# Optimization experiments

Measured on AMD Instinct MI355X. Metric: run time of the kernel, lower is better.

## Reference

```python
import jax, jax.numpy as jnp
import numpy as np

N = 100000   # n_nodes
E = 1600000  # n_edges (avg degree 16)
IN, HID, OUT = 128, 128, 64


def setup_inputs() -> dict:
    key = jax.random.key(0)
    k0, k1, k2, k3 = jax.random.split(key, 4)
    x = jax.random.normal(k0, (N, IN), dtype=jnp.float32)
    edge_index = jax.random.randint(k1, (2, E), 0, N, dtype=jnp.int32)
    # Glorot-ish init for GCNConv weights, zero bias (PyG default bias=True)
    W1 = jax.random.normal(k2, (IN, HID), dtype=jnp.float32) * (1.0 / np.sqrt(IN))
    b1 = jnp.zeros((HID,), dtype=jnp.float32)
    W2 = jax.random.normal(k3, (HID, OUT), dtype=jnp.float32) * (1.0 / np.sqrt(HID))
    b2 = jnp.zeros((OUT,), dtype=jnp.float32)
    return {"x": x, "W1": W1, "b1": b1, "W2": W2, "b2": b2, "edge_index": edge_index}


def gcn_layer(x, W, b, src, dst):
    """PyG GCNConv: add self-loops, symmetric deg^{-1/2} normalization,
    linear transform, scatter-add aggregation at dst, plus bias."""
    n = x.shape[0]
    h = x @ W                                   # [n, d_out]
    loops = jnp.arange(n, dtype=src.dtype)
    s = jnp.concatenate([src, loops])           # sources incl. self-loops
    d = jnp.concatenate([dst, loops])           # targets incl. self-loops
    deg = jax.ops.segment_sum(jnp.ones_like(d, dtype=h.dtype), d, num_segments=n)
    dinv = jnp.where(deg > 0, jax.lax.rsqrt(deg), 0.0)
    norm = dinv[s] * dinv[d]                    # [E+n]
    msg = h[s] * norm[:, None]                  # gather + scale
    out = jax.ops.segment_sum(msg, d, num_segments=n)  # scatter-add
    return out + b


def reference(x, W1, b1, W2, b2, edge_index):
    src, dst = edge_index[0], edge_index[1]
    h = jax.nn.relu(gcn_layer(x, W1, b1, src, dst))
    return gcn_layer(h, W2, b2, src, dst)
```

## Files before the change

kernel.cpp:

```cpp
#include <hip/hip_runtime.h>

#define NNODES 100000
#define NEDGES 1600000
#define IND 128
#define HIDD 128
#define OUTD 64

#define BSHIFT 8
#define BSIZE  256
#define NBUCK  ((NNODES + BSIZE - 1) / BSIZE)
#define SLACK  4800
#define SEG_CAP 5120
#define BIN_EPB 8192
#define BINB   ((NEDGES + BIN_EPB - 1) / BIN_EPB)
#define GEMMB  ((NNODES + 127) / 128)
#define WT2B   ((HIDD * OUTD + 511) / 512)

typedef unsigned int  uint32;
typedef __attribute__((ext_vector_type(8))) short short8;
typedef __attribute__((ext_vector_type(4))) float floatx4;
typedef __attribute__((ext_vector_type(4))) unsigned int uivec4;
typedef __attribute__((ext_vector_type(4))) float fvec4;

__device__ __forceinline__ unsigned short f2bf(float f) {
    union { float f; uint32 u; } x; x.f = f;
    uint32 u = x.u;
    return (unsigned short)((u + 0x7fffu + ((u >> 16) & 1u)) >> 16);
}
__device__ __forceinline__ float bflo(uint32 u) {
    union { uint32 i; float f; } x; x.i = u << 16; return x.f;
}
__device__ __forceinline__ float bfhi(uint32 u) {
    union { uint32 i; float f; } x; x.i = u & 0xffff0000u; return x.f;
}

__launch_bounds__(512)
__global__ void k_bin_gemm(const int* __restrict__ src, const int* __restrict__ dst,
                           int* __restrict__ bcnt, uint32* __restrict__ staging, int e,
                           const float* __restrict__ x, const float* __restrict__ W1,
                           const float* __restrict__ W2, unsigned short* __restrict__ wt2,
                           unsigned short* __restrict__ C, int n) {
    constexpr int K = IND;
    constexpr int KP = K + 8;
    constexpr int M = HIDD;
    constexpr int NT = M / 16;
    __shared__ __align__(16) char smem[2 * 128 * KP * 2];

    const int tid = threadIdx.x;
    const int bid = blockIdx.x;

    if (bid < BINB) {
        int* lh     = (int*)smem;
        int* lstart = lh + NBUCK;
        int* lcur   = lstart + NBUCK;
        int* gres   = lcur + NBUCK;
        int* sbuf   = gres + NBUCK;
        uint32* ent = (uint32*)(sbuf + 512);
        unsigned short* bkt = (unsigned short*)(ent + BIN_EPB);

        for (int i = tid; i < NBUCK; i += 512) lh[i] = 0;
        __syncthreads();

        const int start = bid * BIN_EPB;
        const int end = min(start + BIN_EPB, e);
        const int4* d4 = (const int4*)dst;
        const int4* s4 = (const int4*)src;

        int4 dv[4], sv[4];
        bool val[4];
#pragma unroll
        for (int k = 0; k < 4; k++) {
            int off = start + 4 * (k * 512 + tid);
            val[k] = off < e;
            if (val[k]) { dv[k] = d4[off >> 2]; sv[k] = s4[off >> 2]; }
        }

#pragma unroll
        for (int k = 0; k < 4; k++) {
            if (val[k]) {
                atomicAdd(&lh[dv[k].x >> BSHIFT], 1);
                atomicAdd(&lh[dv[k].y >> BSHIFT], 1);
                atomicAdd(&lh[dv[k].z >> BSHIFT], 1);
                atomicAdd(&lh[dv[k].w >> BSHIFT], 1);
            }
        }
        __syncthreads();

        int vb = (tid < NBUCK) ? lh[tid] : 0;
        sbuf[tid] = vb;
        __syncthreads();
        for (int off = 1; off < 512; off <<= 1) {
            int t = (tid >= off) ? sbuf[tid - off] : 0;
            __syncthreads();
            sbuf[tid] += t;
            __syncthreads();
        }
        if (tid < NBUCK) {
            int ex = sbuf[tid] - vb;
            lstart[tid] = ex;
            lcur[tid]   = ex;
            gres[tid]   = vb ? atomicAdd(&bcnt[tid], vb) : 0;
        }
        __syncthreads();

#pragma unroll
        for (int k = 0; k < 4; k++) {
            if (val[k]) {
                int d, s, b, pos;
                d = dv[k].x; s = sv[k].x; b = d >> BSHIFT;
                pos = atomicAdd(&lcur[b], 1);
                ent[pos] = ((uint32)(d & (BSIZE - 1)) << 17) | (uint32)s;
                bkt[pos] = (unsigned short)b;
                d = dv[k].y; s = sv[k].y; b = d >> BSHIFT;
                pos = atomicAdd(&lcur[b], 1);
                ent[pos] = ((uint32)(d & (BSIZE - 1)) << 17) | (uint32)s;
                bkt[pos] = (unsigned short)b;
                d = dv[k].z; s = sv[k].z; b = d >> BSHIFT;
                pos = atomicAdd(&lcur[b], 1);
                ent[pos] = ((uint32)(d & (BSIZE - 1)) << 17) | (uint32)s;
                bkt[pos] = (unsigned short)b;
                d = dv[k].w; s = sv[k].w; b = d >> BSHIFT;
                pos = atomicAdd(&lcur[b], 1);
                ent[pos] = ((uint32)(d & (BSIZE - 1)) << 17) | (uint32)s;
                bkt[pos] = (unsigned short)b;
            }
        }
        __syncthreads();

        const int total = end - start;
        for (int i = tid; i < total; i += 512) {
            int b = bkt[i];
            int p = gres[b] + (i - lstart[b]);
            if (p < SLACK)
                staging[(size_t)b * SLACK + p] = ent[i];
        }
        return;
    }

    if (bid >= BINB + GEMMB) {
        int idx = (bid - BINB - GEMMB) * 512 + tid;
        if (idx < HIDD * OUTD) {
            int k = idx / OUTD, m = idx - k * OUTD;
            wt2[m * HIDD + k] = f2bf(W2[idx]);
        }
        return;
    }

    unsigned short* Asl = (unsigned short*)smem;
    unsigned short* Wsl = Asl + 128 * KP;

    const int row0 = (bid - BINB) * 128;

    for (int idx = tid; idx < 128 * 128; idx += 512) {
        int k = idx >> 7, m = idx & 127;
        Wsl[m * KP + k] = f2bf(W1[idx]);
    }
    {
        constexpr int F4R = K / 4;
        for (int idx = tid; idx < 128 * F4R; idx += 512) {
            int r = idx / F4R, s = idx - r * F4R;
            int grow = row0 + r; if (grow >= n) grow = n - 1;
            float4 v = *(const float4*)(x + (size_t)grow * K + s * 4);
            uint32 p0 = (uint32)f2bf(v.x) | ((uint32)f2bf(v.y) << 16);
            uint32 p1 = (uint32)f2bf(v.z) | ((uint32)f2bf(v.w) << 16);
            *(uint2*)(Asl + r * KP + s * 4) = make_uint2(p0, p1);
        }
    }
    __syncthreads();

    const int lane = tid & 63;
    const int wave = tid >> 6;
    const int mm = lane & 15;
    const int qq = lane >> 4;

    floatx4 acc[NT];
#pragma unroll
    for (int t = 0; t < NT; t++) acc[t] = (floatx4){0.f, 0.f, 0.f, 0.f};

#pragma unroll
    for (int kc = 0; kc < K / 32; kc++) {
        short8 a = *(const short8*)(Asl + (wave * 16 + mm) * KP + kc * 32 + qq * 8);
#pragma unroll
        for (int t = 0; t < NT; t++) {
            short8 b = *(const short8*)(Wsl + (t * 16 + mm) * KP + kc * 32 + qq * 8);
            acc[t] = __builtin_amdgcn_mfma_f32_16x16x32_bf16(a, b, acc[t], 0, 0, 0);
        }
    }

#pragma unroll
    for (int r = 0; r < 4; r++) {
        int grow = row0 + wave * 16 + qq * 4 + r;
        if (grow < n) {
#pragma unroll
            for (int t = 0; t < NT; t++)
                C[(size_t)grow * M + t * 16 + mm] = f2bf(acc[t][r]);
        }
    }
}

__global__ __launch_bounds__(256)
void k_fill3(const uint32* __restrict__ staging, const int* __restrict__ bcnt,
             int* __restrict__ row_ptr, int* __restrict__ csr_src,
             float* __restrict__ dinv, int n) {
    __shared__ int nc[BSIZE];
    __shared__ int lcur[BSIZE];
    __shared__ int red[256];
    __shared__ int wsum[4];
    __shared__ int seg[SEG_CAP];
    const int b = blockIdx.x;
    const int base = b << BSHIFT;
    const int tid = threadIdx.x;

    nc[tid] = 0;

    int t0 = (tid < b) ? bcnt[tid] : 0;
    int t1 = (tid + 256 < b) ? bcnt[tid + 256] : 0;
    red[tid] = t0 + t1;
    __syncthreads();
    for (int off = 128; off > 0; off >>= 1) {
        if (tid < off) red[tid] += red[tid + off];
        __syncthreads();
    }
    const int r0 = red[0];

    const uint32* st = staging + (size_t)b * SLACK;
    const int cnt = bcnt[b];
    for (int i = tid; i < cnt; i += 256)
        atomicAdd(&nc[st[i] >> 17], 1);
    __syncthreads();

    const int lane = tid & 63;
    const int w = tid >> 6;
    int dg = nc[tid];
    int v = dg;
#pragma unroll
    for (int off = 1; off < 64; off <<= 1) {
        int t = __shfl_up(v, off);
        if (lane >= off) v += t;
    }
    if (lane == 63) wsum[w] = v;
    __syncthreads();
    if (tid == 0) {
        int a = 0;
#pragma unroll
        for (int i = 0; i < 4; i++) { int t = wsum[i]; wsum[i] = a; a += t; }
    }
    __syncthreads();
    const int inc = v + wsum[w];
    const int ex = inc - dg;
    const int vnode = base + tid;
    if (vnode < n) {
        row_ptr[vnode] = r0 + ex;
        dinv[vnode] = rsqrtf((float)(dg + 1));
    }
    lcur[tid] = ex;
    if (b == NBUCK - 1 && tid == 255) row_ptr[n] = r0 + inc;
    __syncthreads();

    for (int i = tid; i < cnt; i += 256) {
        uint32 p = st[i];
        int dl = (int)(p >> 17);
        int s  = (int)(p & 0x1FFFFu);
        int pos = atomicAdd(&lcur[dl], 1);
        if (pos < SEG_CAP) seg[pos] = s;
        else               csr_src[r0 + pos] = s;
    }
    __syncthreads();
    int lim = min(cnt, SEG_CAP);
    for (int i = tid; i < lim; i += 256) csr_src[r0 + i] = seg[i];
}

__launch_bounds__(256)
__global__ void gather_gemm(const unsigned short* __restrict__ h,
                            const int* __restrict__ row_ptr,
                            const int* __restrict__ csr_src,
                            const float* __restrict__ dinv,
                            const float* __restrict__ bias1,
                            const unsigned short* __restrict__ WT2,
                            unsigned short* __restrict__ C2, int n) {
    constexpr int K  = HIDD;
    constexpr int KP = K + 8;
    constexpr int M2 = OUTD;
    __shared__ unsigned short Atl[16 * KP];
    __shared__ unsigned short Wsl[M2 * KP];

    const int tid = threadIdx.x;

    {
        constexpr int SEG = (K * 2) / 16;
        const uint4* srcp = (const uint4*)WT2;
        for (int idx = tid; idx < M2 * SEG; idx += 256) {
            int r = idx / SEG, s = idx - r * SEG;
            *(uint4*)(Wsl + r * KP + s * 8) = srcp[idx];
        }
    }

    const int g = tid >> 4;
    const int l = tid & 15;
    const int v0 = blockIdx.x * 16;
    const int v = v0 + g;

    uint4 pk = make_uint4(0u, 0u, 0u, 0u);
    if (v < n) {
        const float dv = dinv[v];
        float acc[8];
        {
            uint4 u = *(const uint4*)(h + (size_t)v * K + l * 8);
            acc[0] = dv * bflo(u.x); acc[1] = dv * bfhi(u.x);
            acc[2] = dv * bflo(u.y); acc[3] = dv * bfhi(u.y);
            acc[4] = dv * bflo(u.z); acc[5] = dv * bfhi(u.z);
            acc[6] = dv * bflo(u.w); acc[7] = dv * bfhi(u.w);
        }

        int j   = row_ptr[v];
        int end = row_ptr[v + 1];
        for (; j + 3 < end; j += 4) {
            int s0 = csr_src[j];
            int s1 = csr_src[j + 1];
            int s2 = csr_src[j + 2];
            int s3 = csr_src[j + 3];
            float q0 = dinv[s0], q1 = dinv[s1], q2 = dinv[s2], q3 = dinv[s3];
            uint4 u0 = *(const uint4*)(h + (size_t)s0 * K + l * 8);
            uint4 u1 = *(const uint4*)(h + (size_t)s1 * K + l * 8);
            uint4 u2 = *(const uint4*)(h + (size_t)s2 * K + l * 8);
            uint4 u3 = *(const uint4*)(h + (size_t)s3 * K + l * 8);
            acc[0] += (q0 * bflo(u0.x) + q1 * bflo(u1.x)) + (q2 * bflo(u2.x) + q3 * bflo(u3.x));
            acc[1] += (q0 * bfhi(u0.x) + q1 * bfhi(u1.x)) + (q2 * bfhi(u2.x) + q3 * bfhi(u3.x));
            acc[2] += (q0 * bflo(u0.y) + q1 * bflo(u1.y)) + (q2 * bflo(u2.y) + q3 * bflo(u3.y));
            acc[3] += (q0 * bfhi(u0.y) + q1 * bfhi(u1.y)) + (q2 * bfhi(u2.y) + q3 * bfhi(u3.y));
            acc[4] += (q0 * bflo(u0.z) + q1 * bflo(u1.z)) + (q2 * bflo(u2.z) + q3 * bflo(u3.z));
            acc[5] += (q0 * bfhi(u0.z) + q1 * bfhi(u1.z)) + (q2 * bfhi(u2.z) + q3 * bfhi(u3.z));
            acc[6] += (q0 * bflo(u0.w) + q1 * bflo(u1.w)) + (q2 * bflo(u2.w) + q3 * bflo(u3.w));
            acc[7] += (q0 * bfhi(u0.w) + q1 * bfhi(u1.w)) + (q2 * bfhi(u2.w) + q3 * bfhi(u3.w));
        }
        for (; j < end; j++) {
            int s0 = csr_src[j];
            float q0 = dinv[s0];
            uint4 u0 = *(const uint4*)(h + (size_t)s0 * K + l * 8);
            acc[0] += q0 * bflo(u0.x); acc[1] += q0 * bfhi(u0.x);
            acc[2] += q0 * bflo(u0.y); acc[3] += q0 * bfhi(u0.y);
            acc[4] += q0 * bflo(u0.z); acc[5] += q0 * bfhi(u0.z);
            acc[6] += q0 * bflo(u0.w); acc[7] += q0 * bfhi(u0.w);
        }

#pragma unroll
        for (int i = 0; i < 8; i++) {
            acc[i] = fmaxf(acc[i] * dv + bias1[l * 8 + i], 0.0f);
        }
        pk.x = (uint32)f2bf(acc[0]) | ((uint32)f2bf(acc[1]) << 16);
        pk.y = (uint32)f2bf(acc[2]) | ((uint32)f2bf(acc[3]) << 16);
        pk.z = (uint32)f2bf(acc[4]) | ((uint32)f2bf(acc[5]) << 16);
        pk.w = (uint32)f2bf(acc[6]) | ((uint32)f2bf(acc[7]) << 16);
    }
    *(uint4*)(Atl + g * KP + l * 8) = pk;
    __syncthreads();

    const int lane = tid & 63;
    const int wv = tid >> 6;
    const int mm = lane & 15;
    const int qq = lane >> 4;

    floatx4 o = (floatx4){0.f, 0.f, 0.f, 0.f};
#pragma unroll
    for (int kc = 0; kc < K / 32; kc++) {
        short8 a = *(const short8*)(Atl + mm * KP + kc * 32 + qq * 8);
        short8 b = *(const short8*)(Wsl + (wv * 16 + mm) * KP + kc * 32 + qq * 8);
        o = __builtin_amdgcn_mfma_f32_16x16x32_bf16(a, b, o, 0, 0, 0);
    }

#pragma unroll
    for (int r = 0; r < 4; r++) {
        int grow = v0 + qq * 4 + r;
        if (grow < n) {
            float dv2 = dinv[grow];
            C2[(size_t)grow * M2 + wv * 16 + mm] = f2bf(o[r] * dv2);
        }
    }
}

template<int M, bool RELU, bool OBF16>
__launch_bounds__(256)
__global__ void gather_k(const unsigned short* __restrict__ h,
                         const int* __restrict__ row_ptr,
                         const int* __restrict__ csr_src,
                         const float* __restrict__ dinv,
                         const float* __restrict__ bias,
                         void* __restrict__ outp, int n) {
    constexpr int LPG = M / 8;
    constexpr int GPB = 256 / LPG;
    const int g = threadIdx.x / LPG;
    const int l = threadIdx.x % LPG;
    const int v = blockIdx.x * GPB + g;
    if (v >= n) return;

    const float dv = dinv[v];
    float acc[8];
    {
        uint4 u = *(const uint4*)(h + (size_t)v * M + l * 8);
        acc[0] = bflo(u.x); acc[1] = bfhi(u.x);
        acc[2] = bflo(u.y); acc[3] = bfhi(u.y);
        acc[4] = bflo(u.z); acc[5] = bfhi(u.z);
        acc[6] = bflo(u.w); acc[7] = bfhi(u.w);
    }

    int j   = row_ptr[v];
    int end = row_ptr[v + 1];
    for (; j + 3 < end; j += 4) {
        int s0 = csr_src[j];
        int s1 = csr_src[j + 1];
        int s2 = csr_src[j + 2];
        int s3 = csr_src[j + 3];
        uint4 u0 = *(const uint4*)(h + (size_t)s0 * M + l * 8);
        uint4 u1 = *(const uint4*)(h + (size_t)s1 * M + l * 8);
        uint4 u2 = *(const uint4*)(h + (size_t)s2 * M + l * 8);
        uint4 u3 = *(const uint4*)(h + (size_t)s3 * M + l * 8);
        acc[0] += (bflo(u0.x) + bflo(u1.x)) + (bflo(u2.x) + bflo(u3.x));
        acc[1] += (bfhi(u0.x) + bfhi(u1.x)) + (bfhi(u2.x) + bfhi(u3.x));
        acc[2] += (bflo(u0.y) + bflo(u1.y)) + (bflo(u2.y) + bflo(u3.y));
        acc[3] += (bfhi(u0.y) + bfhi(u1.y)) + (bfhi(u2.y) + bfhi(u3.y));
        acc[4] += (bflo(u0.z) + bflo(u1.z)) + (bflo(u2.z) + bflo(u3.z));
        acc[5] += (bfhi(u0.z) + bfhi(u1.z)) + (bfhi(u2.z) + bfhi(u3.z));
        acc[6] += (bflo(u0.w) + bflo(u1.w)) + (bflo(u2.w) + bflo(u3.w));
        acc[7] += (bfhi(u0.w) + bfhi(u1.w)) + (bfhi(u2.w) + bfhi(u3.w));
    }
    for (; j < end; j++) {
        int s0 = csr_src[j];
        uint4 u0 = *(const uint4*)(h + (size_t)s0 * M + l * 8);
        acc[0] += bflo(u0.x); acc[1] += bfhi(u0.x);
        acc[2] += bflo(u0.y); acc[3] += bfhi(u0.y);
        acc[4] += bflo(u0.z); acc[5] += bfhi(u0.z);
        acc[6] += bflo(u0.w); acc[7] += bfhi(u0.w);
    }

#pragma unroll
    for (int i = 0; i < 8; i++) {
        acc[i] = acc[i] * dv + bias[l * 8 + i];
        if (RELU) acc[i] = fmaxf(acc[i], 0.0f);
    }

    if constexpr (OBF16) {
        uivec4 p;
#pragma unroll
        for (int c = 0; c < 4; c++)
            p[c] = (uint32)f2bf(acc[2 * c]) | ((uint32)f2bf(acc[2 * c + 1]) << 16);
        __builtin_nontemporal_store(p,
            (uivec4*)((unsigned short*)outp + (size_t)v * M + l * 8));
    } else {
        float* op = (float*)outp + (size_t)v * M + l * 8;
        fvec4 a0 = {acc[0], acc[1], acc[2], acc[3]};
        fvec4 a1 = {acc[4], acc[5], acc[6], acc[7]};
        __builtin_nontemporal_store(a0, (fvec4*)op);
        __builtin_nontemporal_store(a1, (fvec4*)(op + 4));
    }
}

extern "C" void kernel_launch(void* const* d_in, const int* in_sizes, int n_in,
                              void* d_out, int out_size, void* d_ws, size_t ws_size,
                              hipStream_t stream) {
    const float* x  = (const float*)d_in[0];
    const float* W1 = (const float*)d_in[1];
    const float* b1 = (const float*)d_in[2];
    const float* W2 = (const float*)d_in[3];
    const float* b2 = (const float*)d_in[4];
    const int*   ei = (const int*)d_in[5];
    const int* src = ei;
    const int* dst = ei + NEDGES;
    float* out = (float*)d_out;

    char* ws = (char*)d_ws;
    float*  dinv    = (float*)ws;   ws += (size_t)NNODES * 4;
    int*    row_ptr = (int*)ws;     ws += (size_t)(NNODES + 4) * 4;
    int*    bcnt    = (int*)ws;     ws += 512 * 4;
    unsigned short* wt2 = (unsigned short*)ws;  ws += (size_t)HIDD * OUTD * 2;
    int*    csr_src = (int*)ws;     ws += (size_t)NEDGES * 4;
    uint32* staging = (uint32*)ws;  ws += (size_t)NBUCK * SLACK * 4;
    unsigned short* hbf1 = (unsigned short*)ws; ws += (size_t)NNODES * HIDD * 2;
    unsigned short* hbf2 = (unsigned short*)ws;

    hipMemsetAsync(bcnt, 0, 512 * 4, stream);
    k_bin_gemm<<<BINB + GEMMB + WT2B, 512, 0, stream>>>(
        src, dst, bcnt, staging, NEDGES, x, W1, W2, wt2, hbf1, NNODES);

    k_fill3<<<NBUCK, 256, 0, stream>>>(staging, bcnt, row_ptr, csr_src, dinv, NNODES);

    gather_gemm<<<(NNODES + 15) / 16, 256, 0, stream>>>(
        hbf1, row_ptr, csr_src, dinv, b1, wt2, hbf2, NNODES);

    gather_k<OUTD, false, false><<<(NNODES * (OUTD / 8) + 255) / 256, 256, 0, stream>>>(
        hbf2, row_ptr, csr_src, dinv, b2, out, NNODES);
}
```

Before: 275.4 us.

## Use wave-shuffle scan in binning, vectorize W1 load, widen fill blocks to 512

```diff
diff --git a/kernel.cpp b/kernel.cpp
--- a/kernel.cpp
+++ b/kernel.cpp
@@ -54,8 +54,8 @@
         int* lstart = lh + NBUCK;
         int* lcur   = lstart + NBUCK;
         int* gres   = lcur + NBUCK;
-        int* sbuf   = gres + NBUCK;
-        uint32* ent = (uint32*)(sbuf + 512);
+        int* wsumS  = gres + NBUCK;
+        uint32* ent = (uint32*)(wsumS + 8);
         unsigned short* bkt = (unsigned short*)(ent + BIN_EPB);
 
         for (int i = tid; i < NBUCK; i += 512) lh[i] = 0;
@@ -86,17 +86,25 @@
         }
         __syncthreads();
 
+        const int lane = tid & 63;
+        const int w = tid >> 6;
         int vb = (tid < NBUCK) ? lh[tid] : 0;
-        sbuf[tid] = vb;
-        __syncthreads();
-        for (int off = 1; off < 512; off <<= 1) {
-            int t = (tid >= off) ? sbuf[tid - off] : 0;
-            __syncthreads();
-            sbuf[tid] += t;
-            __syncthreads();
-        }
+        int vsc = vb;
+#pragma unroll
+        for (int off = 1; off < 64; off <<= 1) {
+            int t = __shfl_up(vsc, off);
+            if (lane >= off) vsc += t;
+        }
+        if (lane == 63) wsumS[w] = vsc;
+        __syncthreads();
+        if (tid == 0) {
+            int a = 0;
+#pragma unroll
+            for (int i = 0; i < 8; i++) { int t = wsumS[i]; wsumS[i] = a; a += t; }
+        }
+        __syncthreads();
         if (tid < NBUCK) {
-            int ex = sbuf[tid] - vb;
+            int ex = (vsc + wsumS[w]) - vb;
             lstart[tid] = ex;
             lcur[tid]   = ex;
             gres[tid]   = vb ? atomicAdd(&bcnt[tid], vb) : 0;
@@ -151,9 +159,16 @@
 
     const int row0 = (bid - BINB) * 128;
 
-    for (int idx = tid; idx < 128 * 128; idx += 512) {
-        int k = idx >> 7, m = idx & 127;
-        Wsl[m * KP + k] = f2bf(W1[idx]);
+    {
+        const float4* W14 = (const float4*)W1;
+        for (int idx = tid; idx < 128 * 32; idx += 512) {
+            int k = idx >> 5, m4 = (idx & 31) * 4;
+            float4 wv = W14[idx];
+            Wsl[(m4 + 0) * KP + k] = f2bf(wv.x);
+            Wsl[(m4 + 1) * KP + k] = f2bf(wv.y);
+            Wsl[(m4 + 2) * KP + k] = f2bf(wv.z);
+            Wsl[(m4 + 3) * KP + k] = f2bf(wv.w);
+        }
     }
     {
         constexpr int F4R = K / 4;
@@ -198,26 +213,24 @@
     }
 }
 
-__global__ __launch_bounds__(256)
+__global__ __launch_bounds__(512)
 void k_fill3(const uint32* __restrict__ staging, const int* __restrict__ bcnt,
              int* __restrict__ row_ptr, int* __restrict__ csr_src,
              float* __restrict__ dinv, int n) {
     __shared__ int nc[BSIZE];
     __shared__ int lcur[BSIZE];
-    __shared__ int red[256];
+    __shared__ int red[512];
     __shared__ int wsum[4];
     __shared__ int seg[SEG_CAP];
     const int b = blockIdx.x;
     const int base = b << BSHIFT;
     const int tid = threadIdx.x;
 
-    nc[tid] = 0;
-
-    int t0 = (tid < b) ? bcnt[tid] : 0;
-    int t1 = (tid + 256 < b) ? bcnt[tid + 256] : 0;
-    red[tid] = t0 + t1;
-    __syncthreads();
-    for (int off = 128; off > 0; off >>= 1) {
+    if (tid < BSIZE) nc[tid] = 0;
+
+    red[tid] = (tid < b) ? bcnt[tid] : 0;
+    __syncthreads();
+    for (int off = 256; off > 0; off >>= 1) {
         if (tid < off) red[tid] += red[tid + off];
         __syncthreads();
     }
@@ -225,20 +238,20 @@
 
     const uint32* st = staging + (size_t)b * SLACK;
     const int cnt = bcnt[b];
-    for (int i = tid; i < cnt; i += 256)
+    for (int i = tid; i < cnt; i += 512)
         atomicAdd(&nc[st[i] >> 17], 1);
     __syncthreads();
 
     const int lane = tid & 63;
     const int w = tid >> 6;
-    int dg = nc[tid];
+    int dg = (tid < BSIZE) ? nc[tid] : 0;
     int v = dg;
 #pragma unroll
     for (int off = 1; off < 64; off <<= 1) {
         int t = __shfl_up(v, off);
         if (lane >= off) v += t;
     }
-    if (lane == 63) wsum[w] = v;
+    if (lane == 63 && w < 4) wsum[w] = v;
     __syncthreads();
     if (tid == 0) {
         int a = 0;
@@ -246,18 +259,20 @@
         for (int i = 0; i < 4; i++) { int t = wsum[i]; wsum[i] = a; a += t; }
     }
     __syncthreads();
-    const int inc = v + wsum[w];
-    const int ex = inc - dg;
-    const int vnode = base + tid;
-    if (vnode < n) {
-        row_ptr[vnode] = r0 + ex;
-        dinv[vnode] = rsqrtf((float)(dg + 1));
-    }
-    lcur[tid] = ex;
-    if (b == NBUCK - 1 && tid == 255) row_ptr[n] = r0 + inc;
-    __syncthreads();
-
-    for (int i = tid; i < cnt; i += 256) {
+    if (tid < BSIZE) {
+        const int inc = v + wsum[w];
+        const int ex = inc - dg;
+        const int vnode = base + tid;
+        if (vnode < n) {
+            row_ptr[vnode] = r0 + ex;
+            dinv[vnode] = rsqrtf((float)(dg + 1));
+        }
+        lcur[tid] = ex;
+        if (b == NBUCK - 1 && tid == BSIZE - 1) row_ptr[n] = r0 + inc;
+    }
+    __syncthreads();
+
+    for (int i = tid; i < cnt; i += 512) {
         uint32 p = st[i];
         int dl = (int)(p >> 17);
         int s  = (int)(p & 0x1FFFFu);
@@ -267,7 +282,7 @@
     }
     __syncthreads();
     int lim = min(cnt, SEG_CAP);
-    for (int i = tid; i < lim; i += 256) csr_src[r0 + i] = seg[i];
+    for (int i = tid; i < lim; i += 512) csr_src[r0 + i] = seg[i];
 }
 
 __launch_bounds__(256)
@@ -481,7 +496,7 @@
     k_bin_gemm<<<BINB + GEMMB + WT2B, 512, 0, stream>>>(
         src, dst, bcnt, staging, NEDGES, x, W1, W2, wt2, hbf1, NNODES);
 
-    k_fill3<<<NBUCK, 256, 0, stream>>>(staging, bcnt, row_ptr, csr_src, dinv, NNODES);
+    k_fill3<<<NBUCK, 512, 0, stream>>>(staging, bcnt, row_ptr, csr_src, dinv, NNODES);
 
     gather_gemm<<<(NNODES + 15) / 16, 256, 0, stream>>>(
         hbf1, row_ptr, csr_src, dinv, b1, wt2, hbf2, NNODES);
```

New measurement: 279.0 us. No clear change (+1.3%).
